# Optimization experiments

Measured on AMD Instinct MI355X. Metric: run time of the kernel, lower is better.

## Reference

```python
import jax, jax.numpy as jnp
import numpy as np

B, H, W, C = 32, 56, 56, 256
HEADS, WS, SS, MLP = 8, 7, 3, 1024
N = WS * WS
EPS = 1e-6


def _rel_index():
    # matches source: jnp.meshgrid default 'xy' indexing
    coords = jnp.stack(jnp.meshgrid(jnp.arange(WS), jnp.arange(WS)), axis=0)
    cf = coords.reshape(2, -1)
    rc = (cf[:, :, None] - cf[:, None, :]).transpose(1, 2, 0)
    rc = rc + jnp.array([WS - 1, WS - 1])
    rc = rc.at[:, :, 0].multiply(2 * WS - 1)
    return rc.sum(-1)  # (N, N) int


def _attn_mask():
    # standard shifted-window mask: region ids -> -100 where regions differ
    img = np.zeros((H, W), np.float32)
    cnt = 0
    sl = (slice(0, -WS), slice(-WS, -SS), slice(-SS, None))
    for hs in sl:
        for ws_ in sl:
            img[hs, ws_] = cnt
            cnt += 1
    m = jnp.asarray(img).reshape(H // WS, WS, W // WS, WS)
    m = m.transpose(0, 2, 1, 3).reshape(-1, N)  # (nW, N)
    am = m[:, None, :] - m[:, :, None]
    return jnp.where(am != 0, -100.0, 0.0).astype(jnp.float32)  # (nW, N, N)


def _ln(x, scale, bias):
    mu = x.mean(-1, keepdims=True)
    var = ((x - mu) ** 2).mean(-1, keepdims=True)
    return (x - mu) * jax.lax.rsqrt(var + EPS) * scale + bias


def setup_inputs() -> dict:
    key = jax.random.key(0)
    ks = jax.random.split(key, 8)
    s = 0.02
    return {
        "x": jax.random.normal(ks[0], (B, H * W, C), jnp.float32),
        "ln1_scale": jnp.ones((C,), jnp.float32),
        "ln1_bias": jnp.zeros((C,), jnp.float32),
        "qkv_w": jax.random.normal(ks[1], (C, 3 * C), jnp.float32) * s,
        "qkv_b": jnp.zeros((3 * C,), jnp.float32),
        "proj_w": jax.random.normal(ks[2], (C, C), jnp.float32) * s,
        "proj_b": jnp.zeros((C,), jnp.float32),
        "bias_table": jax.random.normal(ks[3], ((2 * WS - 1) ** 2, HEADS), jnp.float32) * s,
        "ln2_scale": jnp.ones((C,), jnp.float32),
        "ln2_bias": jnp.zeros((C,), jnp.float32),
        "fc1_w": jax.random.normal(ks[4], (C, MLP), jnp.float32) * s,
        "fc1_b": jnp.zeros((MLP,), jnp.float32),
        "fc2_w": jax.random.normal(ks[5], (MLP, C), jnp.float32) * s,
        "fc2_b": jnp.zeros((C,), jnp.float32),
    }


def reference(x, ln1_scale, ln1_bias, qkv_w, qkv_b, proj_w, proj_b, bias_table,
              ln2_scale, ln2_bias, fc1_w, fc1_b, fc2_w, fc2_b):
    Bsz, L, Cdim = x.shape
    d = Cdim // HEADS
    scale = d ** (-0.5)
    nW = (H // WS) * (W // WS)

    shortcut = x
    h = _ln(x, ln1_scale, ln1_bias).reshape(Bsz, H, W, Cdim)
    # cyclic shift
    h = jnp.roll(h, (-SS, -SS), axis=(1, 2))
    # window partition -> (Bsz*nW, N, C)
    win = h.reshape(Bsz, H // WS, WS, W // WS, WS, Cdim)
    win = win.transpose(0, 1, 3, 2, 4, 5).reshape(-1, N, Cdim)

    qkv = (win @ qkv_w + qkv_b).reshape(-1, N, 3, HEADS, d).transpose(2, 0, 3, 1, 4)
    q, k, v = qkv[0] * scale, qkv[1], qkv[2]  # (Bw, heads, N, d)
    attn = q @ k.swapaxes(-2, -1)  # (Bw, heads, N, N)

    rpb = bias_table[_rel_index().reshape(-1)].reshape(N, N, HEADS).transpose(2, 0, 1)
    attn = attn + rpb[None]

    mask = _attn_mask()  # (nW, N, N)
    attn = attn.reshape(Bsz, nW, HEADS, N, N) + mask[None, :, None]
    attn = jax.nn.softmax(attn.reshape(-1, HEADS, N, N), axis=-1)

    out = (attn @ v).swapaxes(1, 2).reshape(-1, N, Cdim)
    out = out @ proj_w + proj_b

    # window reverse + reverse shift
    h = out.reshape(Bsz, H // WS, W // WS, WS, WS, Cdim)
    h = h.transpose(0, 1, 3, 2, 4, 5).reshape(Bsz, H, W, Cdim)
    h = jnp.roll(h, (SS, SS), axis=(1, 2)).reshape(Bsz, L, Cdim)

    x = shortcut + h
    y = _ln(x, ln2_scale, ln2_bias)
    y = jax.nn.gelu(y @ fc1_w + fc1_b) @ fc2_w + fc2_b
    return x + y
```

## Files before the change

kernel.cpp:

```cpp
#include <hip/hip_runtime.h>

typedef unsigned short u16;
typedef short short8v __attribute__((ext_vector_type(8)));
typedef float float4v __attribute__((ext_vector_type(4)));

__device__ __forceinline__ float b2f(u16 u) { return __uint_as_float(((unsigned)u) << 16); }
__device__ __forceinline__ u16 f2b(float f) {
    unsigned i = __float_as_uint(f);
    unsigned r = i + 0x7fffu + ((i >> 16) & 1u);
    return (u16)(r >> 16);
}
__device__ __forceinline__ float gelu_f(float x) {
    float t = x * x;
    float z2 = 1.5957691216057308f * x * __builtin_fmaf(0.044715f, t, 1.0f);
    float e = __expf(z2);
    return x - x * __builtin_amdgcn_rcpf(e + 1.0f);
}

typedef const __attribute__((address_space(1))) unsigned int* gas_ptr;
typedef __attribute__((address_space(3))) unsigned int* las_ptr;
__device__ __forceinline__ void gload16(const u16* g, u16* l) {
    __builtin_amdgcn_global_load_lds((gas_ptr)g, (las_ptr)l, 16, 0, 0);
}

__global__ void transpose_k(const float* __restrict__ in, u16* __restrict__ out, int K, int N) {
    int idx = blockIdx.x * 256 + threadIdx.x;
    if (idx < K * N) {
        int n = idx / K;
        int k = idx - n * K;
        out[idx] = f2b(in[(size_t)k * N + n]);
    }
}

__global__ void build_sadd(const float* __restrict__ btab, u16* __restrict__ tbl) {
    int idx = blockIdx.x * 256 + threadIdx.x;
    int key = idx & 63;
    int q = (idx >> 6) & 63;
    int h = (idx >> 12) & 7;
    int type = idx >> 15;
    float v;
    if (key >= 49 || q >= 49) {
        v = -1e30f;
    } else {
        int qy = q / 7, qx = q - qy * 7;
        int ky = key / 7, kx = key - ky * 7;
        int ridx = (qx - kx + 6) * 13 + (qy - ky + 6);
        v = btab[ridx * 8 + h];
        int rcq = (type & 2) ? (qy < 4 ? 1 : 2) : 0;
        int ccq = (type & 1) ? (qx < 4 ? 1 : 2) : 0;
        int rck = (type & 2) ? (ky < 4 ? 1 : 2) : 0;
        int cck = (type & 1) ? (kx < 4 ? 1 : 2) : 0;
        if (rcq * 3 + ccq != rck * 3 + cck) v += -100.0f;
    }
    tbl[idx] = f2b(v);
}

__global__ __launch_bounds__(256) void ln1_win_kernel(
    const float* __restrict__ x, size_t tok0, const float* __restrict__ sc,
    const float* __restrict__ bi, u16* __restrict__ win) {
    int t = blockIdx.x * 4 + (threadIdx.x >> 6);
    int lane = threadIdx.x & 63;
    int wi = t / 49, p = t - wi * 49;
    int b = wi >> 6, w = wi & 63;
    int wr = w >> 3, wc = w & 7;
    int ii = p / 7, jj = p - ii * 7;
    int r = wr * 7 + ii + 3; if (r >= 56) r -= 56;
    int c = wc * 7 + jj + 3; if (c >= 56) c -= 56;
    size_t off = (tok0 + (size_t)(b * 3136 + r * 56 + c)) * 256 + lane * 4;
    float4 d = *(const float4*)(x + off);
    float v0 = d.x, v1 = d.y, v2 = d.z, v3 = d.w;
    float s = v0 + v1 + v2 + v3;
    float ss = v0 * v0 + v1 * v1 + v2 * v2 + v3 * v3;
#pragma unroll
    for (int o = 32; o; o >>= 1) { s += __shfl_xor(s, o, 64); ss += __shfl_xor(ss, o, 64); }
    float mu = s * (1.0f / 256.0f);
    float rs = rsqrtf(ss * (1.0f / 256.0f) - mu * mu + 1e-6f);
    float4 s4 = *(const float4*)(sc + lane * 4);
    float4 b4 = *(const float4*)(bi + lane * 4);
    ushort4 o4;
    o4.x = f2b((v0 - mu) * rs * s4.x + b4.x);
    o4.y = f2b((v1 - mu) * rs * s4.y + b4.y);
    o4.z = f2b((v2 - mu) * rs * s4.z + b4.z);
    o4.w = f2b((v3 - mu) * rs * s4.w + b4.w);
    *(ushort4*)(win + (size_t)t * 256 + lane * 4) = o4;
}

template <int EPI>
__global__ __launch_bounds__(256) void gemm_bt(
    const u16* __restrict__ A, const u16* __restrict__ Bt, const float* __restrict__ bias,
    const u16* __restrict__ res, void* __restrict__ Cout, int M, int N, int K) {
    __shared__ __align__(16) u16 smem[2][16384];
    int tid = threadIdx.x;
    int bidx = blockIdx.x, bidy = blockIdx.y;
    int nn = gridDim.x, nm = gridDim.y;
    if ((nm & 7) == 0) {
        int d = bidy * nn + bidx;
        int x = d & 7, j = d >> 3;
        int mloc = j / nn;
        bidx = j - mloc * nn;
        bidy = x * (nm >> 3) + mloc;
    }
    int m0 = bidy * 128, n0 = bidx * 128;
    int lane = tid & 63, wave = tid >> 6;
    int wm = (wave >> 1) * 64, wn = (wave & 1) * 64;
    int lrow = lane & 15, qd = lane >> 4;
    int c0 = wave << 2;
    int rsub0 = lane >> 3;
    int kc = (((lane & 7) ^ rsub0) << 3);
    float4v acc[4][4] = {};
    int kTiles = K >> 6;

    const u16* Aps[4];
    const u16* Bps[4];
#pragma unroll
    for (int i = 0; i < 4; ++i) {
        int c = c0 + i;
        int rsub = (c << 3) + rsub0;
        int rA = m0 + rsub; if (rA >= M) rA = M - 1;
        Aps[i] = A + (size_t)rA * K + kc;
        Bps[i] = Bt + (size_t)(n0 + rsub) * K + kc;
    }
#pragma unroll
    for (int i = 0; i < 4; ++i) {
        gload16(Aps[i], &smem[0][(c0 + i) << 9]);
        gload16(Bps[i], &smem[0][8192 + ((c0 + i) << 9)]);
    }
    asm volatile("s_waitcnt vmcnt(0)" ::: "memory");
    __builtin_amdgcn_s_barrier();

    for (int kt = 0; kt < kTiles; ++kt) {
        int cur = kt & 1;
        if (kt + 1 < kTiles) {
            int k0 = (kt + 1) << 6;
#pragma unroll
            for (int i = 0; i < 4; ++i) {
                gload16(Aps[i] + k0, &smem[cur ^ 1][(c0 + i) << 9]);
                gload16(Bps[i] + k0, &smem[cur ^ 1][8192 + ((c0 + i) << 9)]);
            }
        }
        const u16* As = smem[cur];
        const u16* Bs = smem[cur] + 8192;
#pragma unroll
        for (int ks = 0; ks < 64; ks += 32) {
            short8v af[4], bfr[4];
#pragma unroll
            for (int mi = 0; mi < 4; ++mi) {
                int row = wm + mi * 16 + lrow;
                int s = ((ks >> 3) + qd) ^ (row & 7);
                af[mi] = *(const short8v*)&As[row * 64 + (s << 3)];
            }
#pragma unroll
            for (int ni = 0; ni < 4; ++ni) {
                int row = wn + ni * 16 + lrow;
                int s = ((ks >> 3) + qd) ^ (row & 7);
                bfr[ni] = *(const short8v*)&Bs[row * 64 + (s << 3)];
            }
#pragma unroll
            for (int mi = 0; mi < 4; ++mi)
#pragma unroll
                for (int ni = 0; ni < 4; ++ni)
                    acc[mi][ni] = __builtin_amdgcn_mfma_f32_16x16x32_bf16(
                        af[mi], bfr[ni], acc[mi][ni], 0, 0, 0);
        }
        asm volatile("s_waitcnt vmcnt(0)" ::: "memory");
        __builtin_amdgcn_s_barrier();
    }
    if (EPI == 2) {
#pragma unroll
        for (int ni = 0; ni < 4; ++ni) {
            int col = n0 + wn + ni * 16 + lrow;
            float bv = bias[col];
#pragma unroll
            for (int mi = 0; mi < 4; ++mi) {
#pragma unroll
                for (int rr = 0; rr < 4; ++rr) {
                    int row = m0 + wm + mi * 16 + qd * 4 + rr;
                    if (row < M) {
                        float v = acc[mi][ni][rr] + bv + b2f(res[(size_t)row * N + col]);
                        ((float*)Cout)[(size_t)row * N + col] = v;
                    }
                }
            }
        }
    } else {
        u16* ep = (u16*)smem;
#pragma unroll
        for (int ni = 0; ni < 4; ++ni) {
            float bv = bias[n0 + wn + ni * 16 + lrow];
#pragma unroll
            for (int mi = 0; mi < 4; ++mi) {
#pragma unroll
                for (int rr = 0; rr < 4; ++rr) {
                    float v = acc[mi][ni][rr] + bv;
                    if (EPI == 1) v = gelu_f(v);
                    ep[(wm + mi * 16 + qd * 4 + rr) * 136 + wn + ni * 16 + lrow] = f2b(v);
                }
            }
        }
        __syncthreads();
        u16* outp = (u16*)Cout;
#pragma unroll
        for (int j = 0; j < 8; ++j) {
            int slot = j * 256 + tid;
            int row = slot >> 4, cs = (slot & 15) << 3;
            short8v vv = *(const short8v*)&ep[row * 136 + cs];
            int grow = m0 + row;
            if (grow < M)
                *(short8v*)(outp + (size_t)grow * N + n0 + cs) = vv;
        }
    }
}

__global__ __launch_bounds__(256) void attn_kernel(
    const u16* __restrict__ qkv, const u16* __restrict__ sadd, u16* __restrict__ attno) {
    __shared__ __align__(16) u16 lds[4][6272];
    int wave = threadIdx.x >> 6, lane = threadIdx.x & 63;
    u16* Plds = lds[wave];
    u16* Vt = lds[wave] + 4096;
    float* sums = (float*)(lds[wave] + 6144);
    int u = blockIdx.x * 4 + wave;
    int wi = u >> 3, h = u & 7;
    int w = wi & 63;
    int type = (((w >> 3) == 7) ? 2 : 0) | (((w & 7) == 7) ? 1 : 0);
    const u16* base = qkv + (size_t)wi * 49 * 768 + h * 32;
    int lrow = lane & 15, qd = lane >> 4;

#pragma unroll
    for (int z = 0; z < 4; ++z)
        *(short8v*)&Vt[(z * 64 + lane) * 8] = (short8v){0, 0, 0, 0, 0, 0, 0, 0};
    for (int idx = lane; idx < 196; idx += 64) {
        int t = idx >> 2, part = (idx & 3) << 3;
        uint4 vd = *(const uint4*)(base + 512 + (size_t)t * 768 + part);
        const u16* vs = (const u16*)&vd;
#pragma unroll
        for (int e = 0; e < 8; ++e) {
            int c = part + e;
            Vt[c * 64 + ((((t >> 3) ^ (c & 7)) << 3) | (t & 7))] = vs[e];
        }
    }

    short8v qf[4], kf[4];
#pragma unroll
    for (int i = 0; i < 4; ++i) {
        qf[i] = *(const short8v*)(base + (size_t)(16 * i + lrow) * 768 + qd * 8);
        kf[i] = *(const short8v*)(base + 256 + (size_t)(16 * i + lrow) * 768 + qd * 8);
    }
    float4v s[4][4];
#pragma unroll
    for (int i = 0; i < 4; ++i)
#pragma unroll
        for (int j = 0; j < 4; ++j)
            s[i][j] = __builtin_amdgcn_mfma_f32_16x16x32_bf16(
                qf[i], kf[j], (float4v){0.f, 0.f, 0.f, 0.f}, 0, 0, 0);

    const float scale = 0.17677669529663687f;
    const u16* tb = sadd + ((size_t)(type * 8 + h) << 12);
#pragma unroll
    for (int i = 0; i < 4; ++i)
#pragma unroll
        for (int j = 0; j < 4; ++j)
#pragma unroll
            for (int rr = 0; rr < 4; ++rr) {
                int q = 16 * i + qd * 4 + rr, key = 16 * j + lrow;
                float v = s[i][j][rr] * scale + b2f(tb[q * 64 + key]);
                if (j == 3 && lrow > 0) v = -1e30f;
                s[i][j][rr] = v;
            }
    float rmx[4][4];
#pragma unroll
    for (int i = 0; i < 4; ++i)
#pragma unroll
        for (int rr = 0; rr < 4; ++rr) {
            float m = fmaxf(fmaxf(s[i][0][rr], s[i][1][rr]), fmaxf(s[i][2][rr], s[i][3][rr]));
#pragma unroll
            for (int o = 1; o < 16; o <<= 1) m = fmaxf(m, __shfl_xor(m, o, 64));
            rmx[i][rr] = m;
        }
    int hi = lrow >> 3, lo = lrow & 7;
#pragma unroll
    for (int i = 0; i < 4; ++i)
#pragma unroll
        for (int rr = 0; rr < 4; ++rr) {
            int q = 16 * i + qd * 4 + rr;
            float e0 = __expf(s[i][0][rr] - rmx[i][rr]);
            float e1 = __expf(s[i][1][rr] - rmx[i][rr]);
            float e2 = __expf(s[i][2][rr] - rmx[i][rr]);
            float e3 = __expf(s[i][3][rr] - rmx[i][rr]);
            float sm = (e0 + e1) + (e2 + e3);
#pragma unroll
            for (int o = 1; o < 16; o <<= 1) sm += __shfl_xor(sm, o, 64);
            int q64 = q * 64, q7 = q & 7;
            Plds[q64 + ((((0 + hi) ^ q7) << 3) | lo)] = f2b(e0);
            Plds[q64 + ((((2 + hi) ^ q7) << 3) | lo)] = f2b(e1);
            Plds[q64 + ((((4 + hi) ^ q7) << 3) | lo)] = f2b(e2);
            Plds[q64 + ((((6 + hi) ^ q7) << 3) | lo)] = f2b(e3);
            if (lrow == 0) sums[q] = sm;
        }

    float4v o[2][4] = {};
#pragma unroll
    for (int ks = 0; ks < 2; ++ks) {
        short8v av[2], bp[4];
#pragma unroll
        for (int ci = 0; ci < 2; ++ci) {
            int c = 16 * ci + lrow;
            av[ci] = *(const short8v*)&Vt[c * 64 + ((((ks << 2) + qd) ^ (c & 7)) << 3)];
        }
#pragma unroll
        for (int qj = 0; qj < 4; ++qj) {
            int q = 16 * qj + lrow;
            bp[qj] = *(const short8v*)&Plds[q * 64 + ((((ks << 2) + qd) ^ (q & 7)) << 3)];
        }
#pragma unroll
        for (int ci = 0; ci < 2; ++ci)
#pragma unroll
            for (int qj = 0; qj < 4; ++qj)
                o[ci][qj] = __builtin_amdgcn_mfma_f32_16x16x32_bf16(
                    av[ci], bp[qj], o[ci][qj], 0, 0, 0);
    }
#pragma unroll
    for (int qj = 0; qj < 4; ++qj) {
        int q = 16 * qj + lrow;
        if (q < 49) {
            float inv = __builtin_amdgcn_rcpf(sums[q]);
            u16* op = attno + ((size_t)wi * 49 + q) * 256 + h * 32;
#pragma unroll
            for (int ci = 0; ci < 2; ++ci) {
                ushort4 d4;
                d4.x = f2b(o[ci][qj][0] * inv);
                d4.y = f2b(o[ci][qj][1] * inv);
                d4.z = f2b(o[ci][qj][2] * inv);
                d4.w = f2b(o[ci][qj][3] * inv);
                *(ushort4*)(op + 16 * ci + qd * 4) = d4;
            }
        }
    }
}

__global__ __launch_bounds__(256) void scatter_ln2_kernel(
    const float* __restrict__ x, size_t tok0, const u16* __restrict__ projo,
    const float* __restrict__ sc, const float* __restrict__ bi,
    u16* __restrict__ x2, u16* __restrict__ ln2o) {
    int tk = blockIdx.x * 4 + (threadIdx.x >> 6);
    int lane = threadIdx.x & 63;
    int b = tk / 3136, l = tk - b * 3136;
    int r = l / 56, c = l - r * 56;
    int r2 = r + 53; if (r2 >= 56) r2 -= 56;
    int c2 = c + 53; if (c2 >= 56) c2 -= 56;
    int wr = r2 / 7, ri = r2 - wr * 7;
    int wc = c2 / 7, ci = c2 - wc * 7;
    size_t t = ((size_t)(b * 64 + wr * 8 + wc)) * 49 + ri * 7 + ci;
    size_t loff = (size_t)tk * 256 + lane * 4;
    size_t goff = (tok0 + tk) * 256 + lane * 4;
    float4 xd = *(const float4*)(x + goff);
    ushort4 pd = *(const ushort4*)(projo + t * 256 + lane * 4);
    float v0 = xd.x + b2f(pd.x);
    float v1 = xd.y + b2f(pd.y);
    float v2 = xd.z + b2f(pd.z);
    float v3 = xd.w + b2f(pd.w);
    ushort4 o4;
    o4.x = f2b(v0); o4.y = f2b(v1); o4.z = f2b(v2); o4.w = f2b(v3);
    *(ushort4*)(x2 + loff) = o4;
    float s = v0 + v1 + v2 + v3;
    float ss = v0 * v0 + v1 * v1 + v2 * v2 + v3 * v3;
#pragma unroll
    for (int o = 32; o; o >>= 1) { s += __shfl_xor(s, o, 64); ss += __shfl_xor(ss, o, 64); }
    float mu = s * (1.0f / 256.0f);
    float rs = rsqrtf(ss * (1.0f / 256.0f) - mu * mu + 1e-6f);
    float4 s4 = *(const float4*)(sc + lane * 4);
    float4 b4 = *(const float4*)(bi + lane * 4);
    ushort4 n4;
    n4.x = f2b((v0 - mu) * rs * s4.x + b4.x);
    n4.y = f2b((v1 - mu) * rs * s4.y + b4.y);
    n4.z = f2b((v2 - mu) * rs * s4.z + b4.z);
    n4.w = f2b((v3 - mu) * rs * s4.w + b4.w);
    *(ushort4*)(ln2o + loff) = n4;
}

extern "C" void kernel_launch(void* const* d_in, const int* in_sizes, int n_in,
                              void* d_out, int out_size, void* d_ws, size_t ws_size,
                              hipStream_t stream) {
    const float* x     = (const float*)d_in[0];
    const float* ln1s  = (const float*)d_in[1];
    const float* ln1b  = (const float*)d_in[2];
    const float* qkvw  = (const float*)d_in[3];
    const float* qkvb  = (const float*)d_in[4];
    const float* projw = (const float*)d_in[5];
    const float* projb = (const float*)d_in[6];
    const float* btab  = (const float*)d_in[7];
    const float* ln2s  = (const float*)d_in[8];
    const float* ln2b  = (const float*)d_in[9];
    const float* fc1w  = (const float*)d_in[10];
    const float* fc1b  = (const float*)d_in[11];
    const float* fc2w  = (const float*)d_in[12];
    const float* fc2b  = (const float*)d_in[13];
    float* out = (float*)d_out;
    char* ws = (char*)d_ws;

    u16* wt_qkv  = (u16*)(ws + 0);
    u16* wt_proj = (u16*)(ws + 393216);
    u16* wt_fc1  = (u16*)(ws + 524288);
    u16* wt_fc2  = (u16*)(ws + 1048576);
    u16* saddt   = (u16*)(ws + 1572864);
    const size_t base = 1835008;

    build_sadd<<<512, 256, 0, stream>>>(btab, saddt);
    transpose_k<<<768, 256, 0, stream>>>(qkvw, wt_qkv, 256, 768);
    transpose_k<<<256, 256, 0, stream>>>(projw, wt_proj, 256, 256);
    transpose_k<<<1024, 256, 0, stream>>>(fc1w, wt_fc1, 256, 1024);
    transpose_k<<<1024, 256, 0, stream>>>(fc2w, wt_fc2, 1024, 256);

    int NB = 16;
    while (NB > 1 && base + (size_t)NB * 3136 * 3072 > ws_size) NB >>= 1;
    const size_t T = (size_t)NB * 3136;

    u16* regA = (u16*)(ws + base);
    u16* regB = (u16*)(ws + base + T * 512);
    u16* regX = (u16*)(ws + base + T * 512 + T * 2048);

    for (int c0 = 0; c0 < 32; c0 += NB) {
        size_t tok0 = (size_t)c0 * 3136;
        float* outc = out + tok0 * 256;
        int Mc = (int)T;
        int gx = (Mc + 127) / 128;

        ln1_win_kernel<<<Mc / 4, 256, 0, stream>>>(x, tok0, ln1s, ln1b, regA);
        gemm_bt<0><<<dim3(6, gx), 256, 0, stream>>>(regA, wt_qkv, qkvb, nullptr,
                                                    regB, Mc, 768, 256);
        attn_kernel<<<NB * 128, 256, 0, stream>>>(regB, saddt, regA);
        gemm_bt<0><<<dim3(2, gx), 256, 0, stream>>>(regA, wt_proj, projb, nullptr,
                                                    regB, Mc, 256, 256);
        scatter_ln2_kernel<<<Mc / 4, 256, 0, stream>>>(x, tok0, regB, ln2s, ln2b,
                                                       regX, regA);
        gemm_bt<1><<<dim3(8, gx), 256, 0, stream>>>(regA, wt_fc1, fc1b, nullptr,
                                                    regB, Mc, 1024, 256);
        gemm_bt<2><<<dim3(2, gx), 256, 0, stream>>>(regB, wt_fc2, fc2b, regX,
                                                    outc, Mc, 256, 1024);
    }
}
```

Baseline: 704.2 us.

## Shrink GEMM K-tile to 32 and keep two loads in flight with partial waitcnt

The bf16 GEMM main loop now uses 32-wide K tiles instead of 64, which cuts shared memory per block from 64 KiB to about 34 KiB so more blocks can be resident per CU. It also prefetches two tiles ahead and waits with vmcnt(4) rather than draining all loads each step. The XOR swizzle and load mapping are rebuilt for the narrower tile. In exchange there are twice as many loop iterations, each with two barriers and less MFMA work between them.

```diff
diff --git a/kernel.cpp b/kernel.cpp
--- a/kernel.cpp
+++ b/kernel.cpp
@@ -89,7 +89,7 @@
 __global__ __launch_bounds__(256) void gemm_bt(
     const u16* __restrict__ A, const u16* __restrict__ Bt, const float* __restrict__ bias,
     const u16* __restrict__ res, void* __restrict__ Cout, int M, int N, int K) {
-    __shared__ __align__(16) u16 smem[2][16384];
+    __shared__ __align__(16) u16 smem[17408];
     int tid = threadIdx.x;
     int bidx = blockIdx.x, bidy = blockIdx.y;
     int nn = gridDim.x, nm = gridDim.y;
@@ -104,66 +104,72 @@
     int lane = tid & 63, wave = tid >> 6;
     int wm = (wave >> 1) * 64, wn = (wave & 1) * 64;
     int lrow = lane & 15, qd = lane >> 4;
-    int c0 = wave << 2;
-    int rsub0 = lane >> 3;
-    int kc = (((lane & 7) ^ rsub0) << 3);
     float4v acc[4][4] = {};
-    int kTiles = K >> 6;
-
-    const u16* Aps[4];
-    const u16* Bps[4];
-#pragma unroll
-    for (int i = 0; i < 4; ++i) {
-        int c = c0 + i;
-        int rsub = (c << 3) + rsub0;
-        int rA = m0 + rsub; if (rA >= M) rA = M - 1;
-        Aps[i] = A + (size_t)rA * K + kc;
-        Bps[i] = Bt + (size_t)(n0 + rsub) * K + kc;
-    }
-#pragma unroll
-    for (int i = 0; i < 4; ++i) {
-        gload16(Aps[i], &smem[0][(c0 + i) << 9]);
-        gload16(Bps[i], &smem[0][8192 + ((c0 + i) << 9)]);
-    }
-    asm volatile("s_waitcnt vmcnt(0)" ::: "memory");
-    __builtin_amdgcn_s_barrier();
+    int kTiles = K >> 5;
+
+    int row0 = wave * 16 + (lane >> 2);
+    int swz = (lane & 3) ^ ((row0 >> 1) & 3);
+    const u16* pA[2];
+    const u16* pB[2];
+    u16* dA[2];
+    u16* dB[2];
+#pragma unroll
+    for (int j = 0; j < 2; ++j) {
+        int row = row0 + 64 * j;
+        int rA = m0 + row; if (rA >= M) rA = M - 1;
+        pA[j] = A + (size_t)rA * K + swz * 8;
+        pB[j] = Bt + (size_t)(n0 + row) * K + swz * 8;
+        dA[j] = smem + (j * 256 + wave * 64) * 8;
+        dB[j] = smem + 4096 + (j * 256 + wave * 64) * 8;
+    }
+#pragma unroll
+    for (int j = 0; j < 2; ++j) {
+        gload16(pA[j], dA[j]);
+        gload16(pB[j], dB[j]);
+    }
+#pragma unroll
+    for (int j = 0; j < 2; ++j) {
+        gload16(pA[j] + 32, dA[j] + 8192);
+        gload16(pB[j] + 32, dB[j] + 8192);
+    }
 
     for (int kt = 0; kt < kTiles; ++kt) {
-        int cur = kt & 1;
-        if (kt + 1 < kTiles) {
-            int k0 = (kt + 1) << 6;
-#pragma unroll
-            for (int i = 0; i < 4; ++i) {
-                gload16(Aps[i] + k0, &smem[cur ^ 1][(c0 + i) << 9]);
-                gload16(Bps[i] + k0, &smem[cur ^ 1][8192 + ((c0 + i) << 9)]);
+        if (kt + 1 < kTiles)
+            asm volatile("s_waitcnt vmcnt(4)" ::: "memory");
+        else
+            asm volatile("s_waitcnt vmcnt(0)" ::: "memory");
+        __builtin_amdgcn_s_barrier();
+        const u16* As = smem + (kt & 1) * 8192;
+        const u16* Bs = As + 4096;
+        short8v af[4], bfr[4];
+#pragma unroll
+        for (int mi = 0; mi < 4; ++mi) {
+            int row = wm + mi * 16 + lrow;
+            int s = qd ^ ((row >> 1) & 3);
+            af[mi] = *(const short8v*)&As[row * 32 + (s << 3)];
+        }
+#pragma unroll
+        for (int ni = 0; ni < 4; ++ni) {
+            int row = wn + ni * 16 + lrow;
+            int s = qd ^ ((row >> 1) & 3);
+            bfr[ni] = *(const short8v*)&Bs[row * 32 + (s << 3)];
+        }
+#pragma unroll
+        for (int mi = 0; mi < 4; ++mi)
+#pragma unroll
+            for (int ni = 0; ni < 4; ++ni)
+                acc[mi][ni] = __builtin_amdgcn_mfma_f32_16x16x32_bf16(
+                    af[mi], bfr[ni], acc[mi][ni], 0, 0, 0);
+        __builtin_amdgcn_s_barrier();
+        if (kt + 2 < kTiles) {
+            int k0 = (kt + 2) << 5;
+            u16* db = smem + (kt & 1) * 8192;
+#pragma unroll
+            for (int j = 0; j < 2; ++j) {
+                gload16(pA[j] + k0, db + (j * 256 + wave * 64) * 8);
+                gload16(pB[j] + k0, db + 4096 + (j * 256 + wave * 64) * 8);
             }
         }
-        const u16* As = smem[cur];
-        const u16* Bs = smem[cur] + 8192;
-#pragma unroll
-        for (int ks = 0; ks < 64; ks += 32) {
-            short8v af[4], bfr[4];
-#pragma unroll
-            for (int mi = 0; mi < 4; ++mi) {
-                int row = wm + mi * 16 + lrow;
-                int s = ((ks >> 3) + qd) ^ (row & 7);
-                af[mi] = *(const short8v*)&As[row * 64 + (s << 3)];
-            }
-#pragma unroll
-            for (int ni = 0; ni < 4; ++ni) {
-                int row = wn + ni * 16 + lrow;
-                int s = ((ks >> 3) + qd) ^ (row & 7);
-                bfr[ni] = *(const short8v*)&Bs[row * 64 + (s << 3)];
-            }
-#pragma unroll
-            for (int mi = 0; mi < 4; ++mi)
-#pragma unroll
-                for (int ni = 0; ni < 4; ++ni)
-                    acc[mi][ni] = __builtin_amdgcn_mfma_f32_16x16x32_bf16(
-                        af[mi], bfr[ni], acc[mi][ni], 0, 0, 0);
-        }
-        asm volatile("s_waitcnt vmcnt(0)" ::: "memory");
-        __builtin_amdgcn_s_barrier();
     }
     if (EPI == 2) {
 #pragma unroll
@@ -183,7 +189,6 @@
             }
         }
     } else {
-        u16* ep = (u16*)smem;
 #pragma unroll
         for (int ni = 0; ni < 4; ++ni) {
             float bv = bias[n0 + wn + ni * 16 + lrow];
@@ -193,7 +198,7 @@
                 for (int rr = 0; rr < 4; ++rr) {
                     float v = acc[mi][ni][rr] + bv;
                     if (EPI == 1) v = gelu_f(v);
-                    ep[(wm + mi * 16 + qd * 4 + rr) * 136 + wn + ni * 16 + lrow] = f2b(v);
+                    smem[(wm + mi * 16 + qd * 4 + rr) * 136 + wn + ni * 16 + lrow] = f2b(v);
                 }
             }
         }
@@ -203,7 +208,7 @@
         for (int j = 0; j < 8; ++j) {
             int slot = j * 256 + tid;
             int row = slot >> 4, cs = (slot & 15) << 3;
-            short8v vv = *(const short8v*)&ep[row * 136 + cs];
+            short8v vv = *(const short8v*)&smem[row * 136 + cs];
             int grow = m0 + row;
             if (grow < M)
                 *(short8v*)(outp + (size_t)grow * N + n0 + cs) = vv;
```

New measurement: 676.7 us. -3.9%, faster.
